# Performance work log

Measured on AMD Instinct MI355X. Metric: run time of the kernel, lower is better.

## Reference

```python
import jax, jax.numpy as jnp
import numpy as np

DIM = 1024
NUM_HEADS = 16
HEAD_DIM = DIM // NUM_HEADS
TGT_LEN = 4096


def setup_inputs() -> dict:
    key = jax.random.key(0)
    k1, k2, k3 = jax.random.split(key, 3)
    x = jax.random.normal(k1, (TGT_LEN, DIM), dtype=jnp.float32)
    W_in = jax.random.normal(k2, (3 * DIM, DIM), dtype=jnp.float32) * (DIM ** -0.5)
    W_out = jax.random.normal(k3, (DIM, DIM), dtype=jnp.float32) * (DIM ** -0.5)
    return {"x": x, "W_in": W_in, "W_out": W_out, "tgt_len": TGT_LEN}


def reference(x, W_in, W_out, tgt_len):
    # QKV projection (torch Linear: y = x @ W^T)
    qkv = x @ W_in.T  # [T, 3*dim]
    q, k, v = jnp.split(qkv, 3, axis=-1)
    # [T, dim] -> [H, T, hd]
    q = q.reshape(tgt_len, NUM_HEADS, HEAD_DIM).transpose(1, 0, 2)
    k = k.reshape(tgt_len, NUM_HEADS, HEAD_DIM).transpose(1, 0, 2)
    v = v.reshape(tgt_len, NUM_HEADS, HEAD_DIM).transpose(1, 0, 2)
    scaling = HEAD_DIM ** -0.5
    scores = jnp.einsum('htd,hsd->hts', q, k) * scaling  # [H, T, T]
    # joint softmax over the full (T, T) matrix per head (NOT row-wise)
    maxes = jnp.max(scores, axis=(1, 2), keepdims=True)
    x_exp = jnp.exp(scores - maxes)
    probs = x_exp / jnp.sum(x_exp, axis=(1, 2), keepdims=True)
    attn = jnp.einsum('hts,hsd->htd', probs, v)  # [H, T, hd]
    attn = attn.transpose(1, 0, 2).reshape(tgt_len, DIM)
    return attn @ W_out.T
```

## Files before the change

### kernel.cpp

```cpp
#include <hip/hip_runtime.h>

#define TLEN 4096
#define DIM 1024
#define NHEAD 16
#define HDIM 64
#define QKV_COLS (3 * DIM)
#define QSCALE 0.1803368801111244f
#define NCHUNK 2
#define SCHUNK (TLEN / NCHUNK)
#define TB 256
#define NIT (SCHUNK / 64)

typedef __attribute__((ext_vector_type(8))) short short8;
typedef __attribute__((ext_vector_type(4))) float f32x4;

struct alignas(8) s4 { short v[4]; };

__device__ float g_Lsum[NHEAD];

__device__ __forceinline__ unsigned bf16_rtne_bits(float x) {
    unsigned u = __float_as_uint(x);
    return (u + 0x7fffu + ((u >> 16) & 1u)) >> 16;
}

__device__ __forceinline__ void cp16(const short* g, short* l) {
    __builtin_amdgcn_global_load_lds(
        (const __attribute__((address_space(1))) unsigned int*)g,
        (__attribute__((address_space(3))) unsigned int*)l,
        16, 0, 0);
}

__device__ __forceinline__ short8 mk8(unsigned a, unsigned b, unsigned c, unsigned d) {
    union { unsigned u[4]; short8 s; } t;
    t.u[0] = a; t.u[1] = b; t.u[2] = c; t.u[3] = d;
    return t.s;
}

__global__ __launch_bounds__(256) void conv_bf16(
    const float* __restrict__ src, short* __restrict__ dst, int n4)
{
    int i = blockIdx.x * 256 + threadIdx.x;
    if (i < n4) {
        float4 v = ((const float4*)src)[i];
        s4 o;
        o.v[0] = (short)bf16_rtne_bits(v.x);
        o.v[1] = (short)bf16_rtne_bits(v.y);
        o.v[2] = (short)bf16_rtne_bits(v.z);
        o.v[3] = (short)bf16_rtne_bits(v.w);
        ((s4*)dst)[i] = o;
    }
}

__global__ __launch_bounds__(256) void conv_wout(
    const float* __restrict__ src, short* __restrict__ dst)
{
    int i = blockIdx.x * 256 + threadIdx.x;
    float s = 1.0f / g_Lsum[(i & 255) >> 4];
    float4 v = ((const float4*)src)[i];
    s4 o;
    o.v[0] = (short)bf16_rtne_bits(v.x * s);
    o.v[1] = (short)bf16_rtne_bits(v.y * s);
    o.v[2] = (short)bf16_rtne_bits(v.z * s);
    o.v[3] = (short)bf16_rtne_bits(v.w * s);
    ((s4*)dst)[i] = o;
}

__global__ __launch_bounds__(256) void combine(
    const short* __restrict__ p0, const short* __restrict__ p1,
    short* __restrict__ dst, int n4)
{
    int i = blockIdx.x * 256 + threadIdx.x;
    if (i < n4) {
        s4 a = ((const s4*)p0)[i];
        s4 b = ((const s4*)p1)[i];
        s4 o;
#pragma unroll
        for (int m = 0; m < 4; ++m) {
            float fa = __uint_as_float(((unsigned)(unsigned short)a.v[m]) << 16);
            float fb = __uint_as_float(((unsigned)(unsigned short)b.v[m]) << 16);
            o.v[m] = (short)bf16_rtne_bits(fa + fb);
        }
        ((s4*)dst)[i] = o;
    }
}

template <bool QKV_MODE, int BM>
__global__ __launch_bounds__(256) void gemm_bt(
    const short* __restrict__ A, const short* __restrict__ B,
    void* __restrict__ Cout, short* __restrict__ Vout, int M, int N, int K)
{
    constexpr int MI = BM / 32;
    __shared__ __align__(16) short As[BM][32];
    __shared__ __align__(16) short Bs[128][32];
    const int tid  = threadIdx.x;
    const int wv   = tid >> 6, lane = tid & 63;
    const int fr   = lane & 15, quad = lane >> 4;
    const int wm   = (wv >> 1) * (BM / 2), wn = (wv & 1) * 64;
    const int m0 = blockIdx.x * BM, n0 = blockIdx.y * 128;

    if (QKV_MODE && blockIdx.x == 0 && blockIdx.y == 0 && tid < NHEAD)
        g_Lsum[tid] = 0.0f;

    f32x4 acc[MI][4] = {};

    for (int k0 = 0; k0 < K; k0 += 32) {
        __syncthreads();
#pragma unroll
        for (int c = tid; c < 512; c += 256) {
            int row = c >> 2, col = (c & 3) * 8;
            if (BM == 128 || c < BM * 4)
                cp16(A + (size_t)(m0 + row) * K + k0 + col, &As[row][col]);
            cp16(B + (size_t)(n0 + row) * K + k0 + col, &Bs[row][col]);
        }
        __syncthreads();

        short8 af[MI], bfr[4];
#pragma unroll
        for (int i = 0; i < MI; ++i)
            af[i]  = *(const short8*)&As[wm + i * 16 + fr][quad * 8];
#pragma unroll
        for (int j = 0; j < 4; ++j)
            bfr[j] = *(const short8*)&Bs[wn + j * 16 + fr][quad * 8];
#pragma unroll
        for (int i = 0; i < MI; ++i)
#pragma unroll
            for (int j = 0; j < 4; ++j)
                acc[i][j] = __builtin_amdgcn_mfma_f32_16x16x32_bf16(af[i], bfr[j], acc[i][j], 0, 0, 0);
    }

    if (QKV_MODE && n0 >= 2 * DIM) {
#pragma unroll
        for (int i = 0; i < MI; ++i)
#pragma unroll
            for (int j = 0; j < 4; ++j) {
                int n = n0 - 2 * DIM + wn + j * 16 + fr;
                int m = m0 + wm + i * 16 + quad * 4;
                unsigned u0 = bf16_rtne_bits(acc[i][j][0]);
                unsigned u1 = bf16_rtne_bits(acc[i][j][1]);
                unsigned u2 = bf16_rtne_bits(acc[i][j][2]);
                unsigned u3 = bf16_rtne_bits(acc[i][j][3]);
                uint2 pk;
                pk.x = u0 | (u1 << 16);
                pk.y = u2 | (u3 << 16);
                *(uint2*)(Vout + (size_t)n * TLEN + m) = pk;
            }
    } else if (QKV_MODE) {
        const float sc = (n0 < DIM) ? QSCALE : 1.0f;
#pragma unroll
        for (int i = 0; i < MI; ++i)
#pragma unroll
            for (int j = 0; j < 4; ++j)
#pragma unroll
                for (int r = 0; r < 4; ++r) {
                    size_t off = (size_t)(m0 + wm + i * 16 + quad * 4 + r) * N + n0 + wn + j * 16 + fr;
                    ((short*)Cout)[off] = (short)bf16_rtne_bits(acc[i][j][r] * sc);
                }
    } else {
#pragma unroll
        for (int i = 0; i < MI; ++i)
#pragma unroll
            for (int j = 0; j < 4; ++j)
#pragma unroll
                for (int r = 0; r < 4; ++r) {
                    size_t off = (size_t)(m0 + wm + i * 16 + quad * 4 + r) * N + n0 + wn + j * 16 + fr;
                    ((float*)Cout)[off] = acc[i][j][r];
                }
    }
}

__global__ __launch_bounds__(256, 2) void attn_mfma(
    const short* __restrict__ qkvb, const short* __restrict__ vtb,
    short* __restrict__ part)
{
    __shared__ __align__(16) short Ks[2][64][72];
    __shared__ __align__(16) short Vt[2][64][72];
    __shared__ float red[256];

    const int tid = threadIdx.x;
    const int t0 = blockIdx.x * TB;
    const int h  = blockIdx.y;
    const int chunk = blockIdx.z;
    const int srow = tid >> 2;
    const int sch  = (tid & 3) * 16;
    const int wv   = tid >> 6;
    const int lane = tid & 63;
    const int fr   = lane & 15;
    const int quad = lane >> 4;
    const int tb   = wv * 64;

    short8 qf[4][2];
#pragma unroll
    for (int jt = 0; jt < 4; ++jt) {
        const short* qsrc = qkvb + (size_t)(t0 + tb + jt * 16 + fr) * QKV_COLS + h * HDIM + quad * 8;
        qf[jt][0] = *(const short8*)qsrc;
        qf[jt][1] = *(const short8*)(qsrc + 32);
    }

    short8 ones;
#pragma unroll
    for (int m = 0; m < 8; ++m) ones[m] = (short)0x3F80;

    f32x4 oaccT[4][4] = {};
    f32x4 racc[4] = {};

    const int s_begin = chunk * SCHUNK;
    const short* kbase = qkvb + DIM + h * HDIM + sch;
    const short* vbase = vtb + (size_t)(h * HDIM + srow) * TLEN + sch;

    uint4 kA, kB, vA, vB;
    {
        const short* ks = kbase + (size_t)(s_begin + srow) * QKV_COLS;
        kA = *(const uint4*)ks;  kB = *(const uint4*)(ks + 8);
        const short* vs = vbase + s_begin;
        vA = *(const uint4*)vs;  vB = *(const uint4*)(vs + 8);
    }
    *(uint4*)&Ks[0][srow][sch]     = kA;
    *(uint4*)&Ks[0][srow][sch + 8] = kB;
    *(uint4*)&Vt[0][srow][sch]     = vA;
    *(uint4*)&Vt[0][srow][sch + 8] = vB;
    {
        const short* ks = kbase + (size_t)(s_begin + 64 + srow) * QKV_COLS;
        kA = *(const uint4*)ks;  kB = *(const uint4*)(ks + 8);
        const short* vs = vbase + s_begin + 64;
        vA = *(const uint4*)vs;  vB = *(const uint4*)(vs + 8);
    }
    __syncthreads();

    auto step = [&](short (*KsC)[72], short (*VtC)[72],
                    short (*KsN)[72], short (*VtN)[72], int it) {
        if (it + 1 < NIT) {
            *(uint4*)&KsN[srow][sch]     = kA;
            *(uint4*)&KsN[srow][sch + 8] = kB;
            *(uint4*)&VtN[srow][sch]     = vA;
            *(uint4*)&VtN[srow][sch + 8] = vB;
        }
        if (it + 2 < NIT) {
            const int s0n = s_begin + (it + 2) * 64;
            const short* ks = kbase + (size_t)(s0n + srow) * QKV_COLS;
            kA = *(const uint4*)ks;  kB = *(const uint4*)(ks + 8);
            const short* vs = vbase + s0n;
            vA = *(const uint4*)vs;  vB = *(const uint4*)(vs + 8);
        }

        short8 kf[4][2], vf[4][2];
#pragma unroll
        for (int i = 0; i < 4; ++i) {
            kf[i][0] = *(const short8*)&KsC[i * 16 + fr][quad * 8];
            kf[i][1] = *(const short8*)&KsC[i * 16 + fr][32 + quad * 8];
            vf[i][0] = *(const short8*)&VtC[i * 16 + fr][quad * 8];
            vf[i][1] = *(const short8*)&VtC[i * 16 + fr][32 + quad * 8];
        }

#pragma unroll
        for (int jt = 0; jt < 4; ++jt) {
            unsigned w0[4], w1[4];
#pragma unroll
            for (int i = 0; i < 4; ++i) {
                f32x4 acc = {};
                acc = __builtin_amdgcn_mfma_f32_16x16x32_bf16(kf[i][0], qf[jt][0], acc, 0, 0, 0);
                acc = __builtin_amdgcn_mfma_f32_16x16x32_bf16(kf[i][1], qf[jt][1], acc, 0, 0, 0);
                unsigned u0 = __float_as_uint(__builtin_amdgcn_exp2f(acc[0]));
                unsigned u1 = __float_as_uint(__builtin_amdgcn_exp2f(acc[1]));
                unsigned u2 = __float_as_uint(__builtin_amdgcn_exp2f(acc[2]));
                unsigned u3 = __float_as_uint(__builtin_amdgcn_exp2f(acc[3]));
                w0[i] = __builtin_amdgcn_perm(u1, u0, 0x07060302);
                w1[i] = __builtin_amdgcn_perm(u3, u2, 0x07060302);
            }
            auto A0 = __builtin_amdgcn_permlane32_swap(w0[0], w0[1], false, false);
            auto A2 = __builtin_amdgcn_permlane32_swap(w0[2], w0[3], false, false);
            auto B0 = __builtin_amdgcn_permlane32_swap(w1[0], w1[1], false, false);
            auto B2 = __builtin_amdgcn_permlane32_swap(w1[2], w1[3], false, false);
            auto O0 = __builtin_amdgcn_permlane16_swap(A0[0], A0[1], false, false);
            auto O2 = __builtin_amdgcn_permlane16_swap(A2[0], A2[1], false, false);
            auto P0 = __builtin_amdgcn_permlane16_swap(B0[0], B0[1], false, false);
            auto P2 = __builtin_amdgcn_permlane16_swap(B2[0], B2[1], false, false);
            short8 pb0 = mk8(O0[0], P0[0], O0[1], P0[1]);
            short8 pb1 = mk8(O2[0], P2[0], O2[1], P2[1]);

            __builtin_amdgcn_s_setprio(1);
            racc[jt] = __builtin_amdgcn_mfma_f32_16x16x32_bf16(ones, pb0, racc[jt], 0, 0, 0);
            racc[jt] = __builtin_amdgcn_mfma_f32_16x16x32_bf16(ones, pb1, racc[jt], 0, 0, 0);

#pragma unroll
            for (int jd = 0; jd < 4; ++jd) {
                oaccT[jd][jt] = __builtin_amdgcn_mfma_f32_16x16x32_bf16(vf[jd][0], pb0, oaccT[jd][jt], 0, 0, 0);
                oaccT[jd][jt] = __builtin_amdgcn_mfma_f32_16x16x32_bf16(vf[jd][1], pb1, oaccT[jd][jt], 0, 0, 0);
            }
            __builtin_amdgcn_s_setprio(0);
        }
        __syncthreads();
    };

    for (int it = 0; it < NIT; it += 2) {
        step(Ks[0], Vt[0], Ks[1], Vt[1], it);
        step(Ks[1], Vt[1], Ks[0], Vt[0], it + 1);
    }

    short* pc = part + (size_t)chunk * TLEN * DIM;
#pragma unroll
    for (int jt = 0; jt < 4; ++jt)
#pragma unroll
        for (int jd = 0; jd < 4; ++jd) {
            unsigned u0 = bf16_rtne_bits(oaccT[jd][jt][0]);
            unsigned u1 = bf16_rtne_bits(oaccT[jd][jt][1]);
            unsigned u2 = bf16_rtne_bits(oaccT[jd][jt][2]);
            unsigned u3 = bf16_rtne_bits(oaccT[jd][jt][3]);
            uint2 pk;
            pk.x = u0 | (u1 << 16);
            pk.y = u2 | (u3 << 16);
            *(uint2*)(pc + (size_t)(t0 + tb + jt * 16 + fr) * DIM + h * HDIM + jd * 16 + quad * 4) = pk;
        }

    red[tid] = (racc[0][0] + racc[1][0] + racc[2][0] + racc[3][0]) * 0.25f;
    __syncthreads();
    for (int off = 128; off > 0; off >>= 1) {
        if (tid < off) red[tid] += red[tid + off];
        __syncthreads();
    }
    if (tid == 0) atomicAdd(&g_Lsum[h], red[0]);
}

extern "C" void kernel_launch(void* const* d_in, const int* in_sizes, int n_in,
                              void* d_out, int out_size, void* d_ws, size_t ws_size,
                              hipStream_t stream)
{
    const float* x     = (const float*)d_in[0];
    const float* W_in  = (const float*)d_in[1];
    const float* W_out = (const float*)d_in[2];
    float* out = (float*)d_out;

    char* ws = (char*)d_ws;
    short* xb    = (short*)(ws);
    short* wib   = (short*)(ws + (8u << 20));
    short* wob   = (short*)(ws + (14u << 20));
    short* qkvb  = (short*)(ws + (16u << 20));
    short* vtb   = (short*)(ws + (40u << 20));
    short* part  = (short*)(ws + (48u << 20));
    short* attnb = xb;

    conv_bf16<<<(TLEN * DIM / 4 + 255) / 256, 256, 0, stream>>>(x, xb, TLEN * DIM / 4);
    conv_bf16<<<(QKV_COLS * DIM / 4 + 255) / 256, 256, 0, stream>>>(W_in, wib, QKV_COLS * DIM / 4);

    gemm_bt<true, 128><<<dim3(TLEN / 128, QKV_COLS / 128), 256, 0, stream>>>(
        xb, wib, qkvb, vtb, TLEN, QKV_COLS, DIM);

    attn_mfma<<<dim3(TLEN / TB, NHEAD, NCHUNK), 256, 0, stream>>>(qkvb, vtb, part);

    conv_wout<<<(DIM * DIM / 4 + 255) / 256, 256, 0, stream>>>(W_out, wob);

    combine<<<(TLEN * DIM / 4 + 255) / 256, 256, 0, stream>>>(
        part, part + (size_t)TLEN * DIM, attnb, TLEN * DIM / 4);

    gemm_bt<false, 64><<<dim3(TLEN / 64, DIM / 128), 256, 0, stream>>>(
        attnb, wob, out, nullptr, TLEN, DIM, DIM);
}
```

Baseline: 221.3 us.

## Load K and V fragments directly from global memory, dropping LDS staging

```diff
diff --git a/kernel.cpp b/kernel.cpp
--- a/kernel.cpp
+++ b/kernel.cpp
@@ -172,16 +172,12 @@
     const short* __restrict__ qkvb, const short* __restrict__ vtb,
     short* __restrict__ part)
 {
-    __shared__ __align__(16) short Ks[2][64][72];
-    __shared__ __align__(16) short Vt[2][64][72];
     __shared__ float red[256];
 
     const int tid = threadIdx.x;
     const int t0 = blockIdx.x * TB;
     const int h  = blockIdx.y;
     const int chunk = blockIdx.z;
-    const int srow = tid >> 2;
-    const int sch  = (tid & 3) * 16;
     const int wv   = tid >> 6;
     const int lane = tid & 63;
     const int fr   = lane & 15;
@@ -204,51 +200,21 @@
     f32x4 racc[4] = {};
 
     const int s_begin = chunk * SCHUNK;
-    const short* kbase = qkvb + DIM + h * HDIM + sch;
-    const short* vbase = vtb + (size_t)(h * HDIM + srow) * TLEN + sch;
-
-    uint4 kA, kB, vA, vB;
-    {
-        const short* ks = kbase + (size_t)(s_begin + srow) * QKV_COLS;
-        kA = *(const uint4*)ks;  kB = *(const uint4*)(ks + 8);
-        const short* vs = vbase + s_begin;
-        vA = *(const uint4*)vs;  vB = *(const uint4*)(vs + 8);
-    }
-    *(uint4*)&Ks[0][srow][sch]     = kA;
-    *(uint4*)&Ks[0][srow][sch + 8] = kB;
-    *(uint4*)&Vt[0][srow][sch]     = vA;
-    *(uint4*)&Vt[0][srow][sch + 8] = vB;
-    {
-        const short* ks = kbase + (size_t)(s_begin + 64 + srow) * QKV_COLS;
-        kA = *(const uint4*)ks;  kB = *(const uint4*)(ks + 8);
-        const short* vs = vbase + s_begin + 64;
-        vA = *(const uint4*)vs;  vB = *(const uint4*)(vs + 8);
-    }
-    __syncthreads();
-
-    auto step = [&](short (*KsC)[72], short (*VtC)[72],
-                    short (*KsN)[72], short (*VtN)[72], int it) {
-        if (it + 1 < NIT) {
-            *(uint4*)&KsN[srow][sch]     = kA;
-            *(uint4*)&KsN[srow][sch + 8] = kB;
-            *(uint4*)&VtN[srow][sch]     = vA;
-            *(uint4*)&VtN[srow][sch + 8] = vB;
-        }
-        if (it + 2 < NIT) {
-            const int s0n = s_begin + (it + 2) * 64;
-            const short* ks = kbase + (size_t)(s0n + srow) * QKV_COLS;
-            kA = *(const uint4*)ks;  kB = *(const uint4*)(ks + 8);
-            const short* vs = vbase + s0n;
-            vA = *(const uint4*)vs;  vB = *(const uint4*)(vs + 8);
-        }
+    const short* kfb = qkvb + DIM + h * HDIM;
+    const short* vfb = vtb + (size_t)h * HDIM * TLEN;
+
+    for (int it = 0; it < NIT; ++it) {
+        const int s0 = s_begin + it * 64;
 
         short8 kf[4][2], vf[4][2];
 #pragma unroll
         for (int i = 0; i < 4; ++i) {
-            kf[i][0] = *(const short8*)&KsC[i * 16 + fr][quad * 8];
-            kf[i][1] = *(const short8*)&KsC[i * 16 + fr][32 + quad * 8];
-            vf[i][0] = *(const short8*)&VtC[i * 16 + fr][quad * 8];
-            vf[i][1] = *(const short8*)&VtC[i * 16 + fr][32 + quad * 8];
+            const short* kr = kfb + (size_t)(s0 + i * 16 + fr) * QKV_COLS + quad * 8;
+            kf[i][0] = *(const short8*)kr;
+            kf[i][1] = *(const short8*)(kr + 32);
+            const short* vr = vfb + (size_t)(i * 16 + fr) * TLEN + s0 + quad * 8;
+            vf[i][0] = *(const short8*)vr;
+            vf[i][1] = *(const short8*)(vr + 32);
         }
 
 #pragma unroll
@@ -288,12 +254,6 @@
             }
             __builtin_amdgcn_s_setprio(0);
         }
-        __syncthreads();
-    };
-
-    for (int it = 0; it < NIT; it += 2) {
-        step(Ks[0], Vt[0], Ks[1], Vt[1], it);
-        step(Ks[1], Vt[1], Ks[0], Vt[0], it + 1);
     }
 
     short* pc = part + (size_t)chunk * TLEN * DIM;
```

Measured after the change: 267.2 us. +20.8%, slower.
